# Kernel optimization log

Measured on AMD Instinct MI355X. Metric: run time of the kernel, lower is better.

The kernel has to match this reference:

```python
import jax, jax.numpy as jnp
import numpy as np

B, T, I, H = 1024, 512, 256, 256


def setup_inputs() -> dict:
    key = jax.random.key(0)
    k1, k2, k3, k4, k5, k6 = jax.random.split(key, 6)
    bound = 1.0 / np.sqrt(H)  # torch GRUCell init: U(-1/sqrt(H), 1/sqrt(H))
    inp = {
        "input": jax.random.normal(k1, (B, T, I), dtype=jnp.float32),
        "seq_lengths": jax.random.randint(k2, (B,), 0, T, dtype=jnp.int32),
        "W_ih": jax.random.uniform(k3, (3 * H, I), jnp.float32, -bound, bound),
        "W_hh": jax.random.uniform(k4, (3 * H, H), jnp.float32, -bound, bound),
        "b_ih": jax.random.uniform(k5, (3 * H,), jnp.float32, -bound, bound),
        "b_hh": jax.random.uniform(k6, (3 * H,), jnp.float32, -bound, bound),
    }
    return inp


def _gru_last_hidden(x, seq_lengths, W_ih, W_hh, b_ih, b_hh):
    # Precompute all input projections in one big GEMM: [B,T,3H]
    xi = jnp.einsum("bti,gi->btg", x, W_ih) + b_ih
    xi = jnp.swapaxes(xi, 0, 1)  # [T,B,3H] for scan
    h0 = jnp.zeros((x.shape[0], W_hh.shape[1]), dtype=x.dtype)

    def step(carry, inputs):
        h, hn = carry
        xi_t, t = inputs
        gh = h @ W_hh.T + b_hh  # [B,3H]
        xr, xz, xn = jnp.split(xi_t, 3, axis=-1)
        hr, hz, hg = jnp.split(gh, 3, axis=-1)
        r = jax.nn.sigmoid(xr + hr)
        z = jax.nn.sigmoid(xz + hz)
        n = jnp.tanh(xn + r * hg)
        h_new = (1.0 - z) * n + z * h
        mask = (t + 1 <= seq_lengths)[:, None]  # still-observed patients
        hn_new = jnp.where(mask, h_new, hn)
        return (h_new, hn_new), None

    ts = jnp.arange(xi.shape[0], dtype=seq_lengths.dtype)
    (_, hn), _ = jax.lax.scan(step, (h0, h0), (xi, ts))
    return hn


def reference(input, seq_lengths, W_ih, W_hh, b_ih, b_hh):
    return _gru_last_hidden(input, seq_lengths, W_ih, W_hh, b_ih, b_hh)
```

## Files before the change

kernel.cpp:

```cpp
#include <hip/hip_runtime.h>
#include <cstdint>
#include <cstddef>


#define BB 1024
#define TT 512
#define II 256
#define HH 256
#define G3 768

using bfrag = __attribute__((ext_vector_type(8))) short;
using f32x4 = __attribute__((ext_vector_type(4))) float;

static __device__ __forceinline__ unsigned short f2b(float f){
  unsigned u = __builtin_bit_cast(unsigned, f);
  u += 0x7FFFu + ((u >> 16) & 1u);
  return (unsigned short)(u >> 16);
}
static __device__ __forceinline__ float b2f(unsigned short s){
  unsigned u = ((unsigned)s) << 16;
  return __builtin_bit_cast(float, u);
}
static __device__ __forceinline__ float sigm(float x){
  float e = __builtin_amdgcn_exp2f(-1.4426950408889634f * x);
  return __builtin_amdgcn_rcpf(1.0f + e);
}
static __device__ __forceinline__ float tanh_(float x){
  float e = __builtin_amdgcn_exp2f(2.8853900817779268f * x);
  return (e - 1.0f) * __builtin_amdgcn_rcpf(e + 1.0f);
}
static __device__ __forceinline__ float selq(f32x4 v, int q){
  float x01 = (q & 1) ? v[1] : v[0];
  float x23 = (q & 1) ? v[3] : v[2];
  return (q & 2) ? x23 : x01;
}

__global__ void k_init(const float* __restrict__ Wih, const float* __restrict__ Whh,
                       unsigned short* __restrict__ Wihb, unsigned short* __restrict__ Whhb,
                       float* __restrict__ hws, float* __restrict__ out)
{
  int tid = blockIdx.x*256 + threadIdx.x;
  if (tid < 48*8*64*8){
    int j  = tid & 7;
    int L  = (tid >> 3) & 63;
    int ks = (tid >> 9) & 7;
    int nt = tid >> 12;
    int src = (nt*16 + (L&15))*II + ks*32 + (L>>4)*8 + j;
    Wihb[tid] = f2b(Wih[src]);
    Whhb[tid] = f2b(Whh[src]);
  }
  if (tid < BB*HH){ hws[tid] = 0.0f; out[tid] = 0.0f; }
}

__global__ __launch_bounds__(256, 2) void k_proj(
    const float* __restrict__ x, const unsigned short* __restrict__ Wihb,
    const float* __restrict__ bih, unsigned short* __restrict__ xi,
    int t0, int Tc)
{
  __shared__ __align__(16) uint4 wsd[2048];
  const int tid = threadIdx.x, wv = tid>>6, L = tid&63;
  const int lr = L & 15, q = L >> 4;
  const int tpb = Tc >> 4;
  const int tile0 = blockIdx.x*16 + wv*4;

  bfrag a[4][8];
  int bs[4], tls[4];
#pragma unroll
  for (int m=0;m<4;++m){
    int tile = tile0 + m;
    int b = tile / tpb;
    int tl = (tile - b*tpb)*16;
    bs[m]=b; tls[m]=tl;
    const float* xr = x + ((size_t)b*TT + t0 + tl + lr)*II;
#pragma unroll
    for (int ks=0;ks<8;++ks){
      float4 v0 = *(const float4*)(xr + ks*32 + q*8);
      float4 v1 = *(const float4*)(xr + ks*32 + q*8 + 4);
      bfrag f;
      f[0]=(short)f2b(v0.x); f[1]=(short)f2b(v0.y); f[2]=(short)f2b(v0.z); f[3]=(short)f2b(v0.w);
      f[4]=(short)f2b(v1.x); f[5]=(short)f2b(v1.y); f[6]=(short)f2b(v1.z); f[7]=(short)f2b(v1.w);
      a[m][ks]=f;
    }
  }
  for (int nc=0; nc<12; ++nc){
    __syncthreads();
    const uint4* wg = (const uint4*)Wihb + nc*2048;
#pragma unroll
    for (int it=0; it<8; ++it) wsd[it*256+tid] = wg[it*256+tid];
    __syncthreads();
    f32x4 acc[4][4];
#pragma unroll
    for (int nt=0;nt<4;++nt){
      float bv = bih[nc*64 + nt*16 + lr];
#pragma unroll
      for (int m=0;m<4;++m) acc[m][nt] = (f32x4){bv,bv,bv,bv};
    }
#pragma unroll
    for (int ks=0;ks<8;++ks){
#pragma unroll
      for (int nt=0;nt<4;++nt){
        bfrag bf = ((const bfrag*)wsd)[(nt*8+ks)*64 + L];
#pragma unroll
        for (int m=0;m<4;++m)
          acc[m][nt] = __builtin_amdgcn_mfma_f32_16x16x32_bf16(a[m][ks], bf, acc[m][nt], 0,0,0);
      }
    }
#pragma unroll
    for (int m=0;m<4;++m){
      unsigned short* o = xi + ((size_t)(tls[m] + 4*q)*BB + bs[m])*G3 + nc*64 + lr;
#pragma unroll
      for (int nt=0;nt<4;++nt)
#pragma unroll
        for (int r=0;r<4;++r)
          o[(size_t)r*BB*G3 + nt*16] = f2b(acc[m][nt][r]);
    }
  }
}

__global__ __launch_bounds__(512, 2) void k_rec(
    const unsigned short* __restrict__ xi,
    const unsigned short* __restrict__ Whhb,
    const float* __restrict__ bhh,
    const int* __restrict__ seq,
    float* __restrict__ hws,
    float* __restrict__ out,
    int t0, int Tc)
{
  __shared__ __align__(16) unsigned short hsh[2][4*288];
  __shared__ __align__(16) uint4 wlds[8*8*64];
  const int tid = threadIdx.x;
  const int wv = tid >> 6;
  const int L  = tid & 63;
  const int lr = L & 15;
  const int q  = L >> 4;
  const int b0 = blockIdx.x * 4;
  const int c0 = 32*wv + lr, c1 = c0 + 16;

#pragma unroll
  for (int it = 0; it < 8; ++it){
    int idx = it*512 + tid;
    int wvv = idx >> 9, kss = (idx >> 6) & 7, Ls = idx & 63;
    wlds[idx] = ((const uint4*)Whhb)[((33 + 2*wvv)*8 + kss)*64 + Ls];
  }

  bfrag Wf[5][8];
  float bias[6];
#pragma unroll
  for (int g = 0; g < 3; ++g)
#pragma unroll
    for (int p = 0; p < 2; ++p){
      const int f  = g*2 + p;
      const int nt = g*16 + 2*wv + p;
      bias[f] = bhh[g*256 + 32*wv + 16*p + lr];
      if (f < 5){
#pragma unroll
        for (int ks = 0; ks < 8; ++ks)
          Wf[f][ks] = ((const bfrag*)Whhb)[(nt*8 + ks)*64 + L];
      }
    }

  float hp0 = hws[(b0+q)*HH + c0];
  float hp1 = hws[(b0+q)*HH + c1];
  int sl = seq[b0+q] - t0 - 1;
  float* op = out + (size_t)(b0+q)*HH + c0;
  hsh[0][q*288 + c0] = f2b(hp0);
  hsh[0][q*288 + c1] = f2b(hp1);

  const int lo = (b0+q)*G3 + c0;
  const unsigned short* bE = xi;
  const unsigned short* bO = xi + (size_t)BB*G3;
  unsigned short xE0 = bE[lo],     xE1 = bE[lo+16],
                 xE2 = bE[lo+256], xE3 = bE[lo+272],
                 xE4 = bE[lo+512], xE5 = bE[lo+528];
  unsigned short xO0 = bO[lo],     xO1 = bO[lo+16],
                 xO2 = bO[lo+256], xO3 = bO[lo+272],
                 xO4 = bO[lo+512], xO5 = bO[lo+528];
  __syncthreads();

  auto gru_step = [&](int curb, int nxtb,
                      unsigned short X0, unsigned short X1, unsigned short X2,
                      unsigned short X3, unsigned short X4, unsigned short X5,
                      int tcur){
    f32x4 acc[6];
#pragma unroll
    for (int f = 0; f < 6; ++f)
      acc[f] = (f32x4){bias[f], bias[f], bias[f], bias[f]};
#pragma unroll
    for (int ks = 0; ks < 8; ++ks){
      bfrag a  = *(const bfrag*)&hsh[curb][(L & 3)*288 + ks*32 + (L >> 4)*8];
      bfrag b5 = ((const bfrag*)wlds)[(wv*8 + ks)*64 + L];
      acc[0] = __builtin_amdgcn_mfma_f32_16x16x32_bf16(a, Wf[0][ks], acc[0], 0,0,0);
      acc[1] = __builtin_amdgcn_mfma_f32_16x16x32_bf16(a, Wf[1][ks], acc[1], 0,0,0);
      acc[2] = __builtin_amdgcn_mfma_f32_16x16x32_bf16(a, Wf[2][ks], acc[2], 0,0,0);
      acc[3] = __builtin_amdgcn_mfma_f32_16x16x32_bf16(a, Wf[3][ks], acc[3], 0,0,0);
      acc[4] = __builtin_amdgcn_mfma_f32_16x16x32_bf16(a, Wf[4][ks], acc[4], 0,0,0);
      acc[5] = __builtin_amdgcn_mfma_f32_16x16x32_bf16(a, b5,        acc[5], 0,0,0);
    }
    float gr0 = selq(acc[0], q), gr1 = selq(acc[1], q);
    float gz0 = selq(acc[2], q), gz1 = selq(acc[3], q);
    float gn0 = selq(acc[4], q), gn1 = selq(acc[5], q);
    float r0 = sigm(b2f(X0) + gr0), r1 = sigm(b2f(X1) + gr1);
    float z0 = sigm(b2f(X2) + gz0), z1 = sigm(b2f(X3) + gz1);
    float n0 = tanh_(b2f(X4) + r0*gn0), n1 = tanh_(b2f(X5) + r1*gn1);
    float h0 = n0 + z0*(hp0 - n0);
    float h1 = n1 + z1*(hp1 - n1);
    hp0 = h0; hp1 = h1;
    hsh[nxtb][q*288 + c0] = f2b(h0);
    hsh[nxtb][q*288 + c1] = f2b(h1);
    if (tcur == sl){ op[0] = h0; op[16] = h1; }
  };

  const size_t tadv = 2*(size_t)BB*G3;
  for (int tl = 0; tl < Tc; tl += 2){
    gru_step(0, 1, xE0, xE1, xE2, xE3, xE4, xE5, tl);
    if (tl + 2 < Tc) bE += tadv;
    xE0 = bE[lo];     xE1 = bE[lo+16];
    xE2 = bE[lo+256]; xE3 = bE[lo+272];
    xE4 = bE[lo+512]; xE5 = bE[lo+528];
    __syncthreads();
    gru_step(1, 0, xO0, xO1, xO2, xO3, xO4, xO5, tl + 1);
    if (tl + 3 < Tc) bO += tadv;
    xO0 = bO[lo];     xO1 = bO[lo+16];
    xO2 = bO[lo+256]; xO3 = bO[lo+272];
    xO4 = bO[lo+512]; xO5 = bO[lo+528];
    __syncthreads();
  }
  hws[(b0+q)*HH + c0] = hp0;
  hws[(b0+q)*HH + c1] = hp1;
}

extern "C" void kernel_launch(void* const* d_in, const int* in_sizes, int n_in,
                              void* d_out, int out_size, void* d_ws, size_t ws_size,
                              hipStream_t stream)
{
  (void)in_sizes; (void)n_in; (void)out_size;
  const float* x   = (const float*)d_in[0];
  const int*   seq = (const int*)  d_in[1];
  const float* Wih = (const float*)d_in[2];
  const float* Whh = (const float*)d_in[3];
  const float* bih = (const float*)d_in[4];
  const float* bhh = (const float*)d_in[5];
  float* out = (float*)d_out;
  char* ws = (char*)d_ws;
  unsigned short* Whhb = (unsigned short*)(ws);
  unsigned short* Wihb = (unsigned short*)(ws + 393216);
  float* hws = (float*)(ws + (1u<<20));
  unsigned short* xiw = (unsigned short*)(ws + 3u*(1u<<20));
  size_t avail = (ws_size > (size_t)(3u<<20)) ? ws_size - (size_t)(3u<<20) : 0;
  int Tc = TT;
  while (Tc > 16 && (size_t)Tc*BB*G3*2 > avail) Tc >>= 1;

  k_init<<<dim3(1024), dim3(256), 0, stream>>>(Wih, Whh, Wihb, Whhb, hws, out);
  for (int t0 = 0; t0 < TT; t0 += Tc){
    k_proj<<<dim3((BB/256)*Tc), dim3(256), 0, stream>>>(x, Wihb, bih, xiw, t0, Tc);
    k_rec <<<dim3(256), dim3(512), 0, stream>>>(xiw, Whhb, bhh, seq, hws, out, t0, Tc);
  }
}
```

Before: 1.549 ms.

## Keep all recurrent weights in registers, fold r/z biases, prefetch xi earlier

All six W_hh fragments now stay in registers, so the sixth is no longer read from LDS each step. The r and z hidden biases are folded into the input-projection bias in k_proj, so their accumulators start at zero. The xi loads for the next step are issued before the current step's MFMAs to hide global latency. The barriers now wait only on lgkmcnt, not on outstanding global loads. The cost is higher VGPR pressure in k_rec, which could cause spills at the 512-thread, 2-block launch bound.

```diff
diff --git a/kernel.cpp b/kernel.cpp
--- a/kernel.cpp
+++ b/kernel.cpp
@@ -34,9 +34,15 @@
   float x23 = (q & 1) ? v[3] : v[2];
   return (q & 2) ? x23 : x01;
 }
+static __device__ __forceinline__ void barrier_lgkm(){
+  asm volatile("s_waitcnt lgkmcnt(0)" ::: "memory");
+  __builtin_amdgcn_s_barrier();
+}
 
 __global__ void k_init(const float* __restrict__ Wih, const float* __restrict__ Whh,
+                       const float* __restrict__ bih, const float* __restrict__ bhh,
                        unsigned short* __restrict__ Wihb, unsigned short* __restrict__ Whhb,
+                       float* __restrict__ bsum,
                        float* __restrict__ hws, float* __restrict__ out)
 {
   int tid = blockIdx.x*256 + threadIdx.x;
@@ -49,12 +55,13 @@
     Wihb[tid] = f2b(Wih[src]);
     Whhb[tid] = f2b(Whh[src]);
   }
+  if (tid < G3) bsum[tid] = bih[tid] + (tid < 512 ? bhh[tid] : 0.0f);
   if (tid < BB*HH){ hws[tid] = 0.0f; out[tid] = 0.0f; }
 }
 
 __global__ __launch_bounds__(256, 2) void k_proj(
     const float* __restrict__ x, const unsigned short* __restrict__ Wihb,
-    const float* __restrict__ bih, unsigned short* __restrict__ xi,
+    const float* __restrict__ bsum, unsigned short* __restrict__ xi,
     int t0, int Tc)
 {
   __shared__ __align__(16) uint4 wsd[2048];
@@ -91,7 +98,7 @@
     f32x4 acc[4][4];
 #pragma unroll
     for (int nt=0;nt<4;++nt){
-      float bv = bih[nc*64 + nt*16 + lr];
+      float bv = bsum[nc*64 + nt*16 + lr];
 #pragma unroll
       for (int m=0;m<4;++m) acc[m][nt] = (f32x4){bv,bv,bv,bv};
     }
@@ -127,7 +134,6 @@
     int t0, int Tc)
 {
   __shared__ __align__(16) unsigned short hsh[2][4*288];
-  __shared__ __align__(16) uint4 wlds[8*8*64];
   const int tid = threadIdx.x;
   const int wv = tid >> 6;
   const int L  = tid & 63;
@@ -136,33 +142,29 @@
   const int b0 = blockIdx.x * 4;
   const int c0 = 32*wv + lr, c1 = c0 + 16;
 
-#pragma unroll
-  for (int it = 0; it < 8; ++it){
-    int idx = it*512 + tid;
-    int wvv = idx >> 9, kss = (idx >> 6) & 7, Ls = idx & 63;
-    wlds[idx] = ((const uint4*)Whhb)[((33 + 2*wvv)*8 + kss)*64 + Ls];
-  }
-
-  bfrag Wf[5][8];
-  float bias[6];
+  bfrag Wf[6][8];
 #pragma unroll
   for (int g = 0; g < 3; ++g)
 #pragma unroll
     for (int p = 0; p < 2; ++p){
       const int f  = g*2 + p;
       const int nt = g*16 + 2*wv + p;
-      bias[f] = bhh[g*256 + 32*wv + 16*p + lr];
-      if (f < 5){
-#pragma unroll
-        for (int ks = 0; ks < 8; ++ks)
-          Wf[f][ks] = ((const bfrag*)Whhb)[(nt*8 + ks)*64 + L];
-      }
-    }
+#pragma unroll
+      for (int ks = 0; ks < 8; ++ks)
+        Wf[f][ks] = ((const bfrag*)Whhb)[(nt*8 + ks)*64 + L];
+    }
+#pragma unroll
+  for (int f = 0; f < 6; ++f)
+#pragma unroll
+    for (int ks = 0; ks < 8; ++ks)
+      asm volatile("" : "+v"(Wf[f][ks]));
+
+  const float bn0 = bhh[512 + 32*wv + lr];
+  const float bn1 = bhh[512 + 32*wv + 16 + lr];
 
   float hp0 = hws[(b0+q)*HH + c0];
   float hp1 = hws[(b0+q)*HH + c1];
-  int sl = seq[b0+q] - t0 - 1;
-  float* op = out + (size_t)(b0+q)*HH + c0;
+  const int sl = seq[b0+q] - t0 - 1;
   hsh[0][q*288 + c0] = f2b(hp0);
   hsh[0][q*288 + c1] = f2b(hp1);
 
@@ -175,26 +177,28 @@
   unsigned short xO0 = bO[lo],     xO1 = bO[lo+16],
                  xO2 = bO[lo+256], xO3 = bO[lo+272],
                  xO4 = bO[lo+512], xO5 = bO[lo+528];
-  __syncthreads();
+  barrier_lgkm();
 
   auto gru_step = [&](int curb, int nxtb,
                       unsigned short X0, unsigned short X1, unsigned short X2,
                       unsigned short X3, unsigned short X4, unsigned short X5,
                       int tcur){
     f32x4 acc[6];
-#pragma unroll
-    for (int f = 0; f < 6; ++f)
-      acc[f] = (f32x4){bias[f], bias[f], bias[f], bias[f]};
+    acc[0] = (f32x4){0.f,0.f,0.f,0.f};
+    acc[1] = (f32x4){0.f,0.f,0.f,0.f};
+    acc[2] = (f32x4){0.f,0.f,0.f,0.f};
+    acc[3] = (f32x4){0.f,0.f,0.f,0.f};
+    acc[4] = (f32x4){bn0,bn0,bn0,bn0};
+    acc[5] = (f32x4){bn1,bn1,bn1,bn1};
 #pragma unroll
     for (int ks = 0; ks < 8; ++ks){
-      bfrag a  = *(const bfrag*)&hsh[curb][(L & 3)*288 + ks*32 + (L >> 4)*8];
-      bfrag b5 = ((const bfrag*)wlds)[(wv*8 + ks)*64 + L];
+      bfrag a = *(const bfrag*)&hsh[curb][(L & 3)*288 + ks*32 + (L >> 4)*8];
       acc[0] = __builtin_amdgcn_mfma_f32_16x16x32_bf16(a, Wf[0][ks], acc[0], 0,0,0);
       acc[1] = __builtin_amdgcn_mfma_f32_16x16x32_bf16(a, Wf[1][ks], acc[1], 0,0,0);
       acc[2] = __builtin_amdgcn_mfma_f32_16x16x32_bf16(a, Wf[2][ks], acc[2], 0,0,0);
       acc[3] = __builtin_amdgcn_mfma_f32_16x16x32_bf16(a, Wf[3][ks], acc[3], 0,0,0);
       acc[4] = __builtin_amdgcn_mfma_f32_16x16x32_bf16(a, Wf[4][ks], acc[4], 0,0,0);
-      acc[5] = __builtin_amdgcn_mfma_f32_16x16x32_bf16(a, b5,        acc[5], 0,0,0);
+      acc[5] = __builtin_amdgcn_mfma_f32_16x16x32_bf16(a, Wf[5][ks], acc[5], 0,0,0);
     }
     float gr0 = selq(acc[0], q), gr1 = selq(acc[1], q);
     float gz0 = selq(acc[2], q), gz1 = selq(acc[3], q);
@@ -207,23 +211,28 @@
     hp0 = h0; hp1 = h1;
     hsh[nxtb][q*288 + c0] = f2b(h0);
     hsh[nxtb][q*288 + c1] = f2b(h1);
-    if (tcur == sl){ op[0] = h0; op[16] = h1; }
+    if (tcur == sl){
+      float* o = out + (size_t)(b0+q)*HH + c0;
+      o[0] = h0; o[16] = h1;
+    }
   };
 
   const size_t tadv = 2*(size_t)BB*G3;
   for (int tl = 0; tl < Tc; tl += 2){
+    if (tl + 2 < Tc) bE += tadv;
+    unsigned short nE0 = bE[lo],     nE1 = bE[lo+16],
+                   nE2 = bE[lo+256], nE3 = bE[lo+272],
+                   nE4 = bE[lo+512], nE5 = bE[lo+528];
     gru_step(0, 1, xE0, xE1, xE2, xE3, xE4, xE5, tl);
-    if (tl + 2 < Tc) bE += tadv;
-    xE0 = bE[lo];     xE1 = bE[lo+16];
-    xE2 = bE[lo+256]; xE3 = bE[lo+272];
-    xE4 = bE[lo+512]; xE5 = bE[lo+528];
-    __syncthreads();
+    xE0=nE0; xE1=nE1; xE2=nE2; xE3=nE3; xE4=nE4; xE5=nE5;
+    barrier_lgkm();
+    if (tl + 3 < Tc) bO += tadv;
+    unsigned short nO0 = bO[lo],     nO1 = bO[lo+16],
+                   nO2 = bO[lo+256], nO3 = bO[lo+272],
+                   nO4 = bO[lo+512], nO5 = bO[lo+528];
     gru_step(1, 0, xO0, xO1, xO2, xO3, xO4, xO5, tl + 1);
-    if (tl + 3 < Tc) bO += tadv;
-    xO0 = bO[lo];     xO1 = bO[lo+16];
-    xO2 = bO[lo+256]; xO3 = bO[lo+272];
-    xO4 = bO[lo+512]; xO5 = bO[lo+528];
-    __syncthreads();
+    xO0=nO0; xO1=nO1; xO2=nO2; xO3=nO3; xO4=nO4; xO5=nO5;
+    barrier_lgkm();
   }
   hws[(b0+q)*HH + c0] = hp0;
   hws[(b0+q)*HH + c1] = hp1;
@@ -244,15 +253,16 @@
   char* ws = (char*)d_ws;
   unsigned short* Whhb = (unsigned short*)(ws);
   unsigned short* Wihb = (unsigned short*)(ws + 393216);
+  float* bsum = (float*)(ws + 786432);
   float* hws = (float*)(ws + (1u<<20));
   unsigned short* xiw = (unsigned short*)(ws + 3u*(1u<<20));
   size_t avail = (ws_size > (size_t)(3u<<20)) ? ws_size - (size_t)(3u<<20) : 0;
   int Tc = TT;
   while (Tc > 16 && (size_t)Tc*BB*G3*2 > avail) Tc >>= 1;
 
-  k_init<<<dim3(1024), dim3(256), 0, stream>>>(Wih, Whh, Wihb, Whhb, hws, out);
+  k_init<<<dim3(1024), dim3(256), 0, stream>>>(Wih, Whh, bih, bhh, Wihb, Whhb, bsum, hws, out);
   for (int t0 = 0; t0 < TT; t0 += Tc){
-    k_proj<<<dim3((BB/256)*Tc), dim3(256), 0, stream>>>(x, Wihb, bih, xiw, t0, Tc);
+    k_proj<<<dim3((BB/256)*Tc), dim3(256), 0, stream>>>(x, Wihb, bsum, xiw, t0, Tc);
     k_rec <<<dim3(256), dim3(512), 0, stream>>>(xiw, Whhb, bhh, seq, hws, out, t0, Tc);
   }
 }
```

Result: no change. 1.534 ms (-0.9%).
